# Kernel optimization log

Hardware: AMD Instinct MI355X
Metric: run time of the kernel (lower is better)

The kernel has to match this reference:

```python
import jax, jax.numpy as jnp
import numpy as np

D_MODEL = 1024
EXPAND = 2
D_INNER = D_MODEL * EXPAND  # 2048
C = 8
B, T = 4, 2048


def setup_inputs() -> dict:
    key = jax.random.key(0)
    ks = jax.random.split(key, 8)
    x = jax.random.normal(ks[0], (B, T, D_MODEL), jnp.float32)
    # omega init: uniform in [a, b] per the torch code
    a = np.log(1.0 / np.exp(np.log(0.999) / C) - 1.0)
    b = np.log(1.0 / np.exp(np.log(0.9) / C) - 1.0)
    omega = (a + (b - a) * jax.random.uniform(ks[1], (1, 1, D_INNER))).astype(jnp.float32)
    s = 0.02
    Win = (jax.random.normal(ks[2], (2 * D_INNER, D_MODEL)) * s).astype(jnp.float32)   # in_proj, no bias
    Wl = (jax.random.normal(ks[3], (D_INNER, D_INNER)) * s).astype(jnp.float32)        # lambda_proj weight
    bl = jnp.zeros((D_INNER,), jnp.float32)                                            # lambda_proj bias
    Wv = (jax.random.normal(ks[4], (D_INNER, D_INNER)) * s).astype(jnp.float32)        # mixer householder-vector proj
    bv = jnp.zeros((D_INNER,), jnp.float32)
    Wout = (jax.random.normal(ks[5], (D_MODEL, D_INNER)) * s).astype(jnp.float32)      # out_proj, no bias
    return dict(x=x, omega=omega, Win=Win, Wl=Wl, bl=bl, Wv=Wv, bv=bv, Wout=Wout)


def reference(x, omega, Win, Wl, bl, Wv, bv, Wout):
    # in_proj then split into (x, z)
    xz = jnp.einsum('btd,ed->bte', x, Win)              # [B,T,2*D_INNER]
    xi, z = jnp.split(xz, 2, axis=-1)                   # each [B,T,D_INNER]
    # lambda gate (computed for all timesteps at once)
    log_lam = -C * jax.nn.softplus(omega) * jax.nn.sigmoid(jnp.einsum('bti,ji->btj', xi, Wl) + bl)
    lam = jnp.exp(log_lam)                              # [B,T,D_INNER]
    # Householder (rank-1, identity activation) mixer vectors, hoisted out of the scan
    v = jnp.einsum('bti,ji->btj', xi, Wv) + bv          # [B,T,D_INNER]

    h0 = xi[:, 0]                                       # [B,D_INNER]

    def step(h_prev, inp):
        x_t, v_t, lam_t = inp
        vh = jnp.sum(v_t * h_prev, axis=-1, keepdims=True)
        vv = jnp.sum(v_t * v_t, axis=-1, keepdims=True)
        Qh = h_prev - 2.0 * v_t * (vh / vv)             # Householder reflection of h
        h = lam_t * Qh + (1.0 - lam_t) * x_t
        return h, h

    xs = (jnp.swapaxes(xi[:, 1:], 0, 1),                # [T-1,B,D_INNER]
          jnp.swapaxes(v[:, 1:], 0, 1),
          jnp.swapaxes(lam[:, 1:], 0, 1))
    _, hs = jax.lax.scan(step, h0, xs)                  # [T-1,B,D_INNER]
    h = jnp.concatenate([h0[:, None], jnp.swapaxes(hs, 0, 1)], axis=1)  # [B,T,D_INNER]

    return jnp.einsum('bti,di->btd', jax.nn.silu(z) * h, Wout)
```

## Files before the change

### kernel.cpp

```cpp
#include <hip/hip_runtime.h>
#include <cstdint>
#include <cstddef>

typedef unsigned short u16;
typedef __attribute__((ext_vector_type(8))) short s8v;
typedef __attribute__((ext_vector_type(4))) float f4v;
typedef __attribute__((ext_vector_type(2))) float f32x2;

#define D_MODEL 1024
#define D_INNER 2048
#define BT      8192
#define TLEN    2048
#define NBATCH  4

struct alignas(8) U16x4 { u16 x, y, z, w; };

__device__ __forceinline__ u16 f2bf(float f) {
  union { float f; unsigned u; } c; c.f = f;
  unsigned r = c.u + 0x7FFFu + ((c.u >> 16) & 1u);
  return (u16)(r >> 16);
}
__device__ __forceinline__ float bf2f(u16 b) {
  union { unsigned u; float f; } c; c.u = ((unsigned)b) << 16;
  return c.f;
}
__device__ __forceinline__ float blo(unsigned u) {
  union { unsigned u; float f; } c; c.u = u << 16; return c.f;
}
__device__ __forceinline__ float bhi(unsigned u) {
  union { unsigned u; float f; } c; c.u = u & 0xffff0000u; return c.f;
}
__device__ __forceinline__ unsigned pkbf(float lo, float hi) {
  union { float f; unsigned u; } a, b; a.f = lo; b.f = hi;
#if __has_builtin(__builtin_amdgcn_perm)
  return __builtin_amdgcn_perm(b.u + 0x8000u, a.u + 0x8000u, 0x07060302u);
#else
  return ((b.u + 0x8000u) & 0xffff0000u) | ((a.u + 0x8000u) >> 16);
#endif
}

#define DPPADD(x, ctrl) \
  ((x) + __builtin_bit_cast(float, __builtin_amdgcn_update_dpp( \
       0, __builtin_bit_cast(int, (x)), (ctrl), 0xF, 0xF, true)))
__device__ __forceinline__ float wave_sum_dpp(float x) {
  x = DPPADD(x, 0x111);
  x = DPPADD(x, 0x112);
  x = DPPADD(x, 0x114);
  x = DPPADD(x, 0x118);
  x = DPPADD(x, 0x142);
  x = DPPADD(x, 0x143);
  return x;
}

__device__ __forceinline__ void glds16(const u16* g, const u16* lds) {
  __builtin_amdgcn_global_load_lds(
      (const __attribute__((address_space(1))) unsigned int*)(uintptr_t)g,
      (__attribute__((address_space(3))) unsigned int*)(unsigned int)(uintptr_t)lds,
      16, 0, 0);
}

template<int EPI>
__global__ __launch_bounds__(256, 2)
void gemm_nt(const u16* __restrict__ A, const u16* __restrict__ B,
             int M, int N, int K,
             float* __restrict__ Cf, u16* __restrict__ Cb, u16* __restrict__ Cb2,
             const float* __restrict__ bias, const float* __restrict__ sfac,
             const float* __restrict__ bias2)
{
  __shared__ u16 lA[128 * 32];
  __shared__ u16 lB[128 * 32];
  const int tid  = threadIdx.x;
  const int wave = tid >> 6, lane = tid & 63;
  const int wm = wave >> 1, wn = wave & 1;
  const int bm0 = blockIdx.y * 128, bn0 = blockIdx.x * 128;

  const int srow = lane >> 2;
  const int scol = (lane & 3) * 8;
  const u16* pa0 = A + (size_t)(bm0 + wave * 32 + srow) * K + scol;
  const u16* pa1 = pa0 + (size_t)16 * K;
  const u16* pb0 = B + (size_t)(bn0 + wave * 32 + srow) * K + scol;
  const u16* pb1 = pb0 + (size_t)16 * K;
  u16* la0 = lA + (wave * 32) * 32;
  u16* la1 = la0 + 16 * 32;
  u16* lb0 = lB + (wave * 32) * 32;
  u16* lb1 = lb0 + 16 * 32;

  const int fr = lane & 15, kq = lane >> 4;
  const u16* fA = lA + (wm * 64 + fr) * 32 + kq * 8;
  const u16* fB = lB + (wn * 64 + fr) * 32 + kq * 8;

  f4v acc[4][4];
  const f4v zf = {0.f, 0.f, 0.f, 0.f};
  for (int i = 0; i < 4; ++i)
    for (int j = 0; j < 4; ++j)
      acc[i][j] = zf;

  for (int k0 = 0; k0 < K; k0 += 32) {
    glds16(pa0 + k0, la0);
    glds16(pa1 + k0, la1);
    glds16(pb0 + k0, lb0);
    glds16(pb1 + k0, lb1);
    __syncthreads();
    s8v af[4], bfv[4];
#pragma unroll
    for (int i = 0; i < 4; ++i) af[i] = *(const s8v*)(fA + i * 16 * 32);
#pragma unroll
    for (int j = 0; j < 4; ++j) bfv[j] = *(const s8v*)(fB + j * 16 * 32);
#pragma unroll
    for (int i = 0; i < 4; ++i)
#pragma unroll
      for (int j = 0; j < 4; ++j)
        acc[i][j] = __builtin_amdgcn_mfma_f32_16x16x32_bf16(af[i], bfv[j], acc[i][j], 0, 0, 0);
    __syncthreads();
  }

#pragma unroll
  for (int i = 0; i < 4; ++i) {
#pragma unroll
    for (int j = 0; j < 4; ++j) {
#pragma unroll
      for (int r = 0; r < 4; ++r) {
        const int gm = bm0 + wm * 64 + i * 16 + kq * 4 + r;
        const int gn = bn0 + wn * 64 + j * 16 + fr;
        const float val = acc[i][j][r];
        if (EPI == 0) {
          if (gn < D_INNER) {
            Cb[(size_t)gm * D_INNER + gn] = f2bf(val);
          } else {
            const float s = val / (1.f + __expf(-val));
            Cb2[(size_t)gm * D_INNER + (gn - D_INNER)] = f2bf(s);
          }
        } else if (EPI == 4) {
          if (gn < D_INNER) {
            const float pre = val + bias[gn];
            const float sig = 1.f / (1.f + __expf(-pre));
            Cf[(size_t)gm * D_INNER + gn] = __expf(sfac[gn] * sig);
          } else {
            Cb[(size_t)gm * D_INNER + (gn - D_INNER)] = f2bf(val + bias2[gn - D_INNER]);
          }
        } else {
          Cf[(size_t)gm * N + gn] = val;
        }
      }
    }
  }
}

__global__ void conv_bf16_kernel(const float* __restrict__ in, u16* __restrict__ out, int n4)
{
  const int i = blockIdx.x * blockDim.x + threadIdx.x;
  if (i >= n4) return;
  const float4 x = ((const float4*)in)[i];
  U16x4 o; o.x = f2bf(x.x); o.y = f2bf(x.y); o.z = f2bf(x.z); o.w = f2bf(x.w);
  ((U16x4*)out)[i] = o;
}

__global__ void sfac_kernel(const float* __restrict__ omega, float* __restrict__ sfac)
{
  const int i = blockIdx.x * blockDim.x + threadIdx.x;
  if (i < D_INNER) sfac[i] = -8.f * log1pf(expf(omega[i]));
}

__global__ __launch_bounds__(256)
void vscale_kernel(u16* __restrict__ v)
{
  const int row  = blockIdx.x * 4 + (threadIdx.x >> 6);
  const int lane = threadIdx.x & 63;
  uint4* p = (uint4*)(v + (size_t)row * D_INNER + lane * 32);
  uint4 a[4];
#pragma unroll
  for (int i = 0; i < 4; ++i) a[i] = p[i];
  float s = 0.f;
#pragma unroll
  for (int i = 0; i < 4; ++i) {
    const unsigned w[4] = {a[i].x, a[i].y, a[i].z, a[i].w};
#pragma unroll
    for (int j = 0; j < 4; ++j) {
      const float f0 = blo(w[j]), f1 = bhi(w[j]);
      s += f0 * f0 + f1 * f1;
    }
  }
  s += __shfl_down(s, 32); s += __shfl_down(s, 16); s += __shfl_down(s, 8);
  s += __shfl_down(s, 4);  s += __shfl_down(s, 2);  s += __shfl_down(s, 1);
  const float sc = sqrtf(2.f / __shfl(s, 0));
#pragma unroll
  for (int i = 0; i < 4; ++i) {
    const unsigned w[4] = {a[i].x, a[i].y, a[i].z, a[i].w};
    unsigned o[4];
#pragma unroll
    for (int j = 0; j < 4; ++j) o[j] = pkbf(blo(w[j]) * sc, bhi(w[j]) * sc);
    uint4 ov; ov.x = o[0]; ov.y = o[1]; ov.z = o[2]; ov.w = o[3];
    p[i] = ov;
  }
}

__global__ __launch_bounds__(256)
void pairprep_kernel(const u16* __restrict__ vs, const float* __restrict__ lam,
                     const u16* __restrict__ xi, u16* __restrict__ w,
                     f32x2* __restrict__ C12)
{
  const int r = blockIdx.x * 4 + (threadIdx.x >> 6);
  const int lane = threadIdx.x & 63;
  const int b = r >> 10;
  const int t = (r & 1023) * 2;
  const size_t o0 = ((size_t)b * TLEN + t) * D_INNER + (size_t)lane * 32;
  const size_t o1 = o0 + D_INNER;
  const uint4*  pv0 = (const uint4*)(vs + o0);
  const uint4*  pv1 = (const uint4*)(vs + o1);
  const uint4*  px0 = (const uint4*)(xi + o0);
  const float4* pl0 = (const float4*)(lam + o0);
  uint4* pw = (uint4*)(w + (size_t)r * D_INNER + (size_t)lane * 32);
  float c1 = 0.f, c2 = 0.f;
#pragma unroll
  for (int i = 0; i < 4; ++i) {
    const uint4 v0 = pv0[i], v1 = pv1[i], x0 = px0[i];
    const float4 la = pl0[2 * i], lb2 = pl0[2 * i + 1];
    const unsigned v0w[4] = {v0.x, v0.y, v0.z, v0.w};
    const unsigned v1w[4] = {v1.x, v1.y, v1.z, v1.w};
    const unsigned x0w[4] = {x0.x, x0.y, x0.z, x0.w};
    const float lf[8] = {la.x, la.y, la.z, la.w, lb2.x, lb2.y, lb2.z, lb2.w};
    unsigned ow[4];
#pragma unroll
    for (int q = 0; q < 4; ++q) {
      const float va = blo(v0w[q]), vb = bhi(v0w[q]);
      const float ua = blo(v1w[q]), ub = bhi(v1w[q]);
      const float xa = blo(x0w[q]), xb = bhi(x0w[q]);
      ow[q] = pkbf(ua * lf[2 * q], ub * lf[2 * q + 1]);
      c1 += blo(ow[q]) * va + bhi(ow[q]) * vb;
      c2 += ua * (1.f - lf[2 * q]) * xa + ub * (1.f - lf[2 * q + 1]) * xb;
    }
    uint4 o; o.x = ow[0]; o.y = ow[1]; o.z = ow[2]; o.w = ow[3];
    pw[i] = o;
  }
  c1 = wave_sum_dpp(c1);
  c2 = wave_sum_dpp(c2);
  if (lane == 63) { f32x2 cc; cc.x = c1; cc.y = c2; C12[r] = cc; }
}

struct Pair {
  uint4 v0, v1, w, x0, x1, z0, z1;
  float4 l0a, l0b, l1a, l1b;
  f32x2 c;
};

__global__ __launch_bounds__(256, 1)
void scan2_kernel(const u16* __restrict__ xi, const u16* __restrict__ sz,
                  const u16* __restrict__ vs, const float* __restrict__ lam,
                  const u16* __restrict__ whalf, const f32x2* __restrict__ C12,
                  u16* __restrict__ gh)
{
  const int b = blockIdx.x, tid = threadIdx.x;
  const int wave = tid >> 6, lane = tid & 63;
  const size_t base = (size_t)b * TLEN * D_INNER + (size_t)tid * 8;
  const size_t wb0  = (size_t)(b * 1024) * D_INNER + (size_t)tid * 8;
  const int cb0 = b * 1024;
  __shared__ __attribute__((aligned(16))) float rP[2][4], rQ[2][4];

  auto load_pair = [&](int t) {
    Pair p;
    const size_t o0 = base + (size_t)t * D_INNER;
    const size_t o1 = o0 + D_INNER;
    p.v0 = *(const uint4*)(vs + o0);
    p.v1 = *(const uint4*)(vs + o1);
    p.w  = *(const uint4*)(whalf + wb0 + (size_t)(t >> 1) * D_INNER);
    p.x0 = *(const uint4*)(xi + o0);
    p.x1 = *(const uint4*)(xi + o1);
    p.z0 = *(const uint4*)(sz + o0);
    p.z1 = *(const uint4*)(sz + o1);
    const float4* l0p = (const float4*)(lam + o0);
    p.l0a = l0p[0]; p.l0b = l0p[1];
    const float4* l1p = (const float4*)(lam + o1);
    p.l1a = l1p[0]; p.l1b = l1p[1];
    p.c = C12[cb0 + (t >> 1)];
    return p;
  };

  float h[8];
  {
    const uint4 x0 = *(const uint4*)(xi + base);
    const uint4 z0 = *(const uint4*)(sz + base);
    const unsigned xw[4] = {x0.x, x0.y, x0.z, x0.w};
    const unsigned zw[4] = {z0.x, z0.y, z0.z, z0.w};
    unsigned ow[4];
#pragma unroll
    for (int p = 0; p < 4; ++p) {
      h[2*p]   = blo(xw[p]);
      h[2*p+1] = bhi(xw[p]);
      ow[p] = pkbf(blo(zw[p]) * h[2*p], bhi(zw[p]) * h[2*p+1]);
    }
    uint4 out; out.x = ow[0]; out.y = ow[1]; out.z = ow[2]; out.w = ow[3];
    *(uint4*)(gh + base) = out;
  }

  {
    const size_t o = base + D_INNER;
    const uint4 v1v = *(const uint4*)(vs + o);
    const uint4 x1v = *(const uint4*)(xi + o);
    const uint4 z1v = *(const uint4*)(sz + o);
    const float4* lp = (const float4*)(lam + o);
    const float4 la = lp[0], lb2 = lp[1];
    const unsigned vw[4] = {v1v.x, v1v.y, v1v.z, v1v.w};
    float vf[8];
    float P0 = 0.f, P1 = 0.f;
#pragma unroll
    for (int p = 0; p < 4; ++p) {
      vf[2*p]   = blo(vw[p]);
      vf[2*p+1] = bhi(vw[p]);
      P0 = __builtin_fmaf(vf[2*p],   h[2*p],   P0);
      P1 = __builtin_fmaf(vf[2*p+1], h[2*p+1], P1);
    }
    float P = wave_sum_dpp(P0 + P1);
    if (lane == 63) rP[0][wave] = P;
    asm volatile("s_waitcnt lgkmcnt(0)\n\ts_barrier" ::: "memory");
    const float4 sp = *(const float4*)rP[0];
    const float a = (sp.x + sp.y) + (sp.z + sp.w);
    const float lf[8] = {la.x, la.y, la.z, la.w, lb2.x, lb2.y, lb2.z, lb2.w};
    const unsigned xw[4] = {x1v.x, x1v.y, x1v.z, x1v.w};
    const unsigned zw[4] = {z1v.x, z1v.y, z1v.z, z1v.w};
    unsigned ow[4];
#pragma unroll
    for (int p = 0; p < 4; ++p) {
      const float X0 = blo(xw[p]), X1 = bhi(xw[p]);
      const float t0 = __builtin_fmaf(vf[2*p],   -a, h[2*p]);
      const float t1 = __builtin_fmaf(vf[2*p+1], -a, h[2*p+1]);
      h[2*p]   = __builtin_fmaf(lf[2*p],   t0 - X0, X0);
      h[2*p+1] = __builtin_fmaf(lf[2*p+1], t1 - X1, X1);
      ow[p] = pkbf(blo(zw[p]) * h[2*p], bhi(zw[p]) * h[2*p+1]);
    }
    uint4 out; out.x = ow[0]; out.y = ow[1]; out.z = ow[2]; out.w = ow[3];
    *(uint4*)(gh + o) = out;
  }

  auto round = [&](const Pair& p, int t) {
    const int par = (t >> 1) & 1;
    const unsigned vw[4] = {p.v0.x, p.v0.y, p.v0.z, p.v0.w};
    const unsigned ww[4] = {p.w.x, p.w.y, p.w.z, p.w.w};
    float vf[8];
    float P0 = 0.f, P1 = 0.f, Q0 = 0.f, Q1 = 0.f;
#pragma unroll
    for (int q = 0; q < 4; ++q) {
      vf[2*q]   = blo(vw[q]);
      vf[2*q+1] = bhi(vw[q]);
      const float wa = blo(ww[q]), wb = bhi(ww[q]);
      P0 = __builtin_fmaf(vf[2*q],   h[2*q],   P0);
      P1 = __builtin_fmaf(vf[2*q+1], h[2*q+1], P1);
      Q0 = __builtin_fmaf(wa, h[2*q],   Q0);
      Q1 = __builtin_fmaf(wb, h[2*q+1], Q1);
    }
    float P = wave_sum_dpp(P0 + P1);
    float Q = wave_sum_dpp(Q0 + Q1);
    if (lane == 63) { rP[par][wave] = P; rQ[par][wave] = Q; }
    asm volatile("s_waitcnt lgkmcnt(0)\n\ts_barrier" ::: "memory");
    const float4 sp = *(const float4*)rP[par];
    const float4 sq = *(const float4*)rQ[par];
    const float a0 = (sp.x + sp.y) + (sp.z + sp.w);
    const float a1 = __builtin_fmaf(-a0, p.c.x, (sq.x + sq.y) + (sq.z + sq.w) + p.c.y);
    const float lf0[8] = {p.l0a.x, p.l0a.y, p.l0a.z, p.l0a.w,
                          p.l0b.x, p.l0b.y, p.l0b.z, p.l0b.w};
    const float lf1[8] = {p.l1a.x, p.l1a.y, p.l1a.z, p.l1a.w,
                          p.l1b.x, p.l1b.y, p.l1b.z, p.l1b.w};
    const unsigned v1w[4] = {p.v1.x, p.v1.y, p.v1.z, p.v1.w};
    const unsigned xw0[4] = {p.x0.x, p.x0.y, p.x0.z, p.x0.w};
    const unsigned xw1[4] = {p.x1.x, p.x1.y, p.x1.z, p.x1.w};
    const unsigned zw0[4] = {p.z0.x, p.z0.y, p.z0.z, p.z0.w};
    const unsigned zw1[4] = {p.z1.x, p.z1.y, p.z1.z, p.z1.w};
    unsigned ow0[4], ow1[4];
#pragma unroll
    for (int q = 0; q < 4; ++q) {
      const float A0 = blo(xw0[q]), A1 = bhi(xw0[q]);
      const float B0 = blo(xw1[q]), B1 = bhi(xw1[q]);
      float t0 = __builtin_fmaf(vf[2*q],   -a0, h[2*q]);
      float t1 = __builtin_fmaf(vf[2*q+1], -a0, h[2*q+1]);
      t0 = __builtin_fmaf(lf0[2*q],   t0 - A0, A0);
      t1 = __builtin_fmaf(lf0[2*q+1], t1 - A1, A1);
      ow0[q] = pkbf(blo(zw0[q]) * t0, bhi(zw0[q]) * t1);
      const float u0 = __builtin_fmaf(blo(v1w[q]), -a1, t0);
      const float u1 = __builtin_fmaf(bhi(v1w[q]), -a1, t1);
      h[2*q]   = __builtin_fmaf(lf1[2*q],   u0 - B0, B0);
      h[2*q+1] = __builtin_fmaf(lf1[2*q+1], u1 - B1, B1);
      ow1[q] = pkbf(blo(zw1[q]) * h[2*q], bhi(zw1[q]) * h[2*q+1]);
    }
    const size_t oo = base + (size_t)t * D_INNER;
    uint4 o0; o0.x = ow0[0]; o0.y = ow0[1]; o0.z = ow0[2]; o0.w = ow0[3];
    uint4 o1; o1.x = ow1[0]; o1.y = ow1[1]; o1.z = ow1[2]; o1.w = ow1[3];
    *(uint4*)(gh + oo) = o0;
    *(uint4*)(gh + oo + D_INNER) = o1;
  };

  Pair A = load_pair(2);
  __builtin_amdgcn_sched_barrier(0);
  Pair B = load_pair(4);
  __builtin_amdgcn_sched_barrier(0);
  for (int t = 2; t <= 2038; t += 4) {
    Pair An = load_pair(t + 4);
    __builtin_amdgcn_sched_barrier(0);
    round(A, t);
    A = An;
    Pair Bn = load_pair(t + 6);
    __builtin_amdgcn_sched_barrier(0);
    round(B, t + 2);
    B = Bn;
  }
  {
    Pair An = load_pair(2046);
    __builtin_amdgcn_sched_barrier(0);
    round(A, 2042);
    round(B, 2044);
    round(An, 2046);
  }
}

extern "C" void kernel_launch(void* const* d_in, const int* in_sizes, int n_in,
                              void* d_out, int out_size, void* d_ws, size_t ws_size,
                              hipStream_t stream)
{
  const float* x     = (const float*)d_in[0];
  const float* omega = (const float*)d_in[1];
  const float* Win   = (const float*)d_in[2];
  const float* Wl    = (const float*)d_in[3];
  const float* bl    = (const float*)d_in[4];
  const float* Wv    = (const float*)d_in[5];
  const float* bv    = (const float*)d_in[6];
  const float* Wout  = (const float*)d_in[7];
  float* out = (float*)d_out;
  (void)in_sizes; (void)n_in; (void)out_size; (void)ws_size;

  size_t off = 0;
  auto carve = [&](size_t bytes) -> void* {
    void* r = (char*)d_ws + off;
    off += (bytes + 255) & ~(size_t)255;
    return r;
  };
  u16*  x_bf    = (u16*)carve((size_t)BT * D_MODEL * 2);
  u16*  Win_bf  = (u16*)carve((size_t)2 * D_INNER * D_MODEL * 2);
  u16*  Wl_bf   = (u16*)carve((size_t)D_INNER * D_INNER * 2);
  u16*  Wv_bf   = (u16*)carve((size_t)D_INNER * D_INNER * 2);
  u16*  Wout_bf = (u16*)carve((size_t)D_MODEL * D_INNER * 2);
  u16*  xi_bf   = (u16*)carve((size_t)BT * D_INNER * 2);
  u16*  sz_bf   = (u16*)carve((size_t)BT * D_INNER * 2);
  u16*  v_bf    = (u16*)carve((size_t)BT * D_INNER * 2);
  u16*  gh_bf   = (u16*)carve((size_t)BT * D_INNER * 2);
  float* lam    = (float*)carve((size_t)BT * D_INNER * 4);
  float* sfac   = (float*)carve((size_t)D_INNER * 4);
  f32x2* C12    = (f32x2*)carve((size_t)(BT / 2) * 8);
  u16*  whalf   = x_bf;

  conv_bf16_kernel<<<(BT * D_MODEL / 4 + 255) / 256, 256, 0, stream>>>(x, x_bf, BT * D_MODEL / 4);
  conv_bf16_kernel<<<(2 * D_INNER * D_MODEL / 4 + 255) / 256, 256, 0, stream>>>(Win, Win_bf, 2 * D_INNER * D_MODEL / 4);
  conv_bf16_kernel<<<(D_INNER * D_INNER / 4 + 255) / 256, 256, 0, stream>>>(Wl, Wl_bf, D_INNER * D_INNER / 4);
  conv_bf16_kernel<<<(D_INNER * D_INNER / 4 + 255) / 256, 256, 0, stream>>>(Wv, Wv_bf, D_INNER * D_INNER / 4);
  conv_bf16_kernel<<<(D_MODEL * D_INNER / 4 + 255) / 256, 256, 0, stream>>>(Wout, Wout_bf, D_MODEL * D_INNER / 4);
  sfac_kernel<<<(D_INNER + 255) / 256, 256, 0, stream>>>(omega, sfac);

  gemm_nt<0><<<dim3(4096 / 128, BT / 128), 256, 0, stream>>>(
      x_bf, Win_bf, BT, 4096, D_MODEL, nullptr, xi_bf, sz_bf, nullptr, nullptr, nullptr);
  gemm_nt<4><<<dim3(4096 / 128, BT / 128), 256, 0, stream>>>(
      xi_bf, Wl_bf, BT, 4096, D_INNER, lam, v_bf, nullptr, bl, sfac, bv);
  vscale_kernel<<<BT / 4, 256, 0, stream>>>(v_bf);
  pairprep_kernel<<<BT / 2 / 4, 256, 0, stream>>>(v_bf, lam, xi_bf, whalf, C12);
  scan2_kernel<<<NBATCH, 256, 0, stream>>>(xi_bf, sz_bf, v_bf, lam, whalf, C12, gh_bf);
  gemm_nt<3><<<dim3(D_MODEL / 128, BT / 128), 256, 0, stream>>>(
      gh_bf, Wout_bf, BT, D_MODEL, D_INNER, out, nullptr, nullptr, nullptr, nullptr, nullptr);
}
```

Before: 1.265 ms.

## Shrink scan memory traffic: bf16 one-minus-lambda, drop w buffer, move z-gate out

The lambda GEMM epilogue now stores m = 1 - lambda (via -expm1) as bf16 instead of fp32 lambda, which halves that buffer. The serial scan no longer reads z, fp32 lambda or the precomputed w buffer; it rebuilds w from v1 and m in registers and writes raw h. A new elementwise zmul kernel applies the silu(z) gate afterwards. The aim is to cut per-step bytes loaded in the latency-bound 4-block scan, at the cost of an extra full pass over gh and sz and some bf16 rounding of m.

```diff
diff --git a/kernel.cpp b/kernel.cpp
--- a/kernel.cpp
+++ b/kernel.cpp
@@ -19,10 +19,6 @@
   union { float f; unsigned u; } c; c.f = f;
   unsigned r = c.u + 0x7FFFu + ((c.u >> 16) & 1u);
   return (u16)(r >> 16);
-}
-__device__ __forceinline__ float bf2f(u16 b) {
-  union { unsigned u; float f; } c; c.u = ((unsigned)b) << 16;
-  return c.f;
 }
 __device__ __forceinline__ float blo(unsigned u) {
   union { unsigned u; float f; } c; c.u = u << 16; return c.f;
@@ -134,7 +130,8 @@
           if (gn < D_INNER) {
             const float pre = val + bias[gn];
             const float sig = 1.f / (1.f + __expf(-pre));
-            Cf[(size_t)gm * D_INNER + gn] = __expf(sfac[gn] * sig);
+            const float m = -expm1f(sfac[gn] * sig);
+            Cb2[(size_t)gm * D_INNER + gn] = f2bf(m);
           } else {
             Cb[(size_t)gm * D_INNER + (gn - D_INNER)] = f2bf(val + bias2[gn - D_INNER]);
           }
@@ -195,9 +192,8 @@
 }
 
 __global__ __launch_bounds__(256)
-void pairprep_kernel(const u16* __restrict__ vs, const float* __restrict__ lam,
-                     const u16* __restrict__ xi, u16* __restrict__ w,
-                     f32x2* __restrict__ C12)
+void pairprep_kernel(const u16* __restrict__ vs, const u16* __restrict__ mb,
+                     const u16* __restrict__ xi, f32x2* __restrict__ C12)
 {
   const int r = blockIdx.x * 4 + (threadIdx.x >> 6);
   const int lane = threadIdx.x & 63;
@@ -205,54 +201,64 @@
   const int t = (r & 1023) * 2;
   const size_t o0 = ((size_t)b * TLEN + t) * D_INNER + (size_t)lane * 32;
   const size_t o1 = o0 + D_INNER;
-  const uint4*  pv0 = (const uint4*)(vs + o0);
-  const uint4*  pv1 = (const uint4*)(vs + o1);
-  const uint4*  px0 = (const uint4*)(xi + o0);
-  const float4* pl0 = (const float4*)(lam + o0);
-  uint4* pw = (uint4*)(w + (size_t)r * D_INNER + (size_t)lane * 32);
+  const uint4* pv0 = (const uint4*)(vs + o0);
+  const uint4* pv1 = (const uint4*)(vs + o1);
+  const uint4* px0 = (const uint4*)(xi + o0);
+  const uint4* pm0 = (const uint4*)(mb + o0);
   float c1 = 0.f, c2 = 0.f;
 #pragma unroll
   for (int i = 0; i < 4; ++i) {
-    const uint4 v0 = pv0[i], v1 = pv1[i], x0 = px0[i];
-    const float4 la = pl0[2 * i], lb2 = pl0[2 * i + 1];
+    const uint4 v0 = pv0[i], v1 = pv1[i], x0 = px0[i], m0 = pm0[i];
     const unsigned v0w[4] = {v0.x, v0.y, v0.z, v0.w};
     const unsigned v1w[4] = {v1.x, v1.y, v1.z, v1.w};
     const unsigned x0w[4] = {x0.x, x0.y, x0.z, x0.w};
-    const float lf[8] = {la.x, la.y, la.z, la.w, lb2.x, lb2.y, lb2.z, lb2.w};
-    unsigned ow[4];
+    const unsigned m0w[4] = {m0.x, m0.y, m0.z, m0.w};
 #pragma unroll
     for (int q = 0; q < 4; ++q) {
       const float va = blo(v0w[q]), vb = bhi(v0w[q]);
       const float ua = blo(v1w[q]), ub = bhi(v1w[q]);
       const float xa = blo(x0w[q]), xb = bhi(x0w[q]);
-      ow[q] = pkbf(ua * lf[2 * q], ub * lf[2 * q + 1]);
-      c1 += blo(ow[q]) * va + bhi(ow[q]) * vb;
-      c2 += ua * (1.f - lf[2 * q]) * xa + ub * (1.f - lf[2 * q + 1]) * xb;
-    }
-    uint4 o; o.x = ow[0]; o.y = ow[1]; o.z = ow[2]; o.w = ow[3];
-    pw[i] = o;
+      const float ma = blo(m0w[q]), mbv = bhi(m0w[q]);
+      const float wa = __builtin_fmaf(-ua, ma, ua);
+      const float wb = __builtin_fmaf(-ub, mbv, ub);
+      c1 += wa * va + wb * vb;
+      c2 += ua * (ma * xa) + ub * (mbv * xb);
+    }
   }
   c1 = wave_sum_dpp(c1);
   c2 = wave_sum_dpp(c2);
   if (lane == 63) { f32x2 cc; cc.x = c1; cc.y = c2; C12[r] = cc; }
 }
 
+__global__ void zmul_kernel(u16* __restrict__ gh, const u16* __restrict__ sz, int n8)
+{
+  const int i = blockIdx.x * blockDim.x + threadIdx.x;
+  if (i >= n8) return;
+  const uint4 hv = ((const uint4*)gh)[i];
+  const uint4 zv = ((const uint4*)sz)[i];
+  const unsigned hw[4] = {hv.x, hv.y, hv.z, hv.w};
+  const unsigned zw[4] = {zv.x, zv.y, zv.z, zv.w};
+  unsigned ow[4];
+#pragma unroll
+  for (int q = 0; q < 4; ++q)
+    ow[q] = pkbf(blo(zw[q]) * blo(hw[q]), bhi(zw[q]) * bhi(hw[q]));
+  uint4 o; o.x = ow[0]; o.y = ow[1]; o.z = ow[2]; o.w = ow[3];
+  ((uint4*)gh)[i] = o;
+}
+
 struct Pair {
-  uint4 v0, v1, w, x0, x1, z0, z1;
-  float4 l0a, l0b, l1a, l1b;
+  uint4 v0, v1, x0, x1, m0, m1;
   f32x2 c;
 };
 
 __global__ __launch_bounds__(256, 1)
-void scan2_kernel(const u16* __restrict__ xi, const u16* __restrict__ sz,
-                  const u16* __restrict__ vs, const float* __restrict__ lam,
-                  const u16* __restrict__ whalf, const f32x2* __restrict__ C12,
-                  u16* __restrict__ gh)
+void scan2_kernel(const u16* __restrict__ xi, const u16* __restrict__ vs,
+                  const u16* __restrict__ mb, const f32x2* __restrict__ C12,
+                  u16* __restrict__ hb)
 {
   const int b = blockIdx.x, tid = threadIdx.x;
   const int wave = tid >> 6, lane = tid & 63;
   const size_t base = (size_t)b * TLEN * D_INNER + (size_t)tid * 8;
-  const size_t wb0  = (size_t)(b * 1024) * D_INNER + (size_t)tid * 8;
   const int cb0 = b * 1024;
   __shared__ __attribute__((aligned(16))) float rP[2][4], rQ[2][4];
 
@@ -262,15 +268,10 @@
     const size_t o1 = o0 + D_INNER;
     p.v0 = *(const uint4*)(vs + o0);
     p.v1 = *(const uint4*)(vs + o1);
-    p.w  = *(const uint4*)(whalf + wb0 + (size_t)(t >> 1) * D_INNER);
     p.x0 = *(const uint4*)(xi + o0);
     p.x1 = *(const uint4*)(xi + o1);
-    p.z0 = *(const uint4*)(sz + o0);
-    p.z1 = *(const uint4*)(sz + o1);
-    const float4* l0p = (const float4*)(lam + o0);
-    p.l0a = l0p[0]; p.l0b = l0p[1];
-    const float4* l1p = (const float4*)(lam + o1);
-    p.l1a = l1p[0]; p.l1b = l1p[1];
+    p.m0 = *(const uint4*)(mb + o0);
+    p.m1 = *(const uint4*)(mb + o1);
     p.c = C12[cb0 + (t >> 1)];
     return p;
   };
@@ -278,27 +279,20 @@
   float h[8];
   {
     const uint4 x0 = *(const uint4*)(xi + base);
-    const uint4 z0 = *(const uint4*)(sz + base);
     const unsigned xw[4] = {x0.x, x0.y, x0.z, x0.w};
-    const unsigned zw[4] = {z0.x, z0.y, z0.z, z0.w};
-    unsigned ow[4];
 #pragma unroll
     for (int p = 0; p < 4; ++p) {
       h[2*p]   = blo(xw[p]);
       h[2*p+1] = bhi(xw[p]);
-      ow[p] = pkbf(blo(zw[p]) * h[2*p], bhi(zw[p]) * h[2*p+1]);
-    }
-    uint4 out; out.x = ow[0]; out.y = ow[1]; out.z = ow[2]; out.w = ow[3];
-    *(uint4*)(gh + base) = out;
+    }
+    *(uint4*)(hb + base) = x0;
   }
 
   {
     const size_t o = base + D_INNER;
     const uint4 v1v = *(const uint4*)(vs + o);
     const uint4 x1v = *(const uint4*)(xi + o);
-    const uint4 z1v = *(const uint4*)(sz + o);
-    const float4* lp = (const float4*)(lam + o);
-    const float4 la = lp[0], lb2 = lp[1];
+    const uint4 m1v = *(const uint4*)(mb + o);
     const unsigned vw[4] = {v1v.x, v1v.y, v1v.z, v1v.w};
     float vf[8];
     float P0 = 0.f, P1 = 0.f;
@@ -314,34 +308,40 @@
     asm volatile("s_waitcnt lgkmcnt(0)\n\ts_barrier" ::: "memory");
     const float4 sp = *(const float4*)rP[0];
     const float a = (sp.x + sp.y) + (sp.z + sp.w);
-    const float lf[8] = {la.x, la.y, la.z, la.w, lb2.x, lb2.y, lb2.z, lb2.w};
     const unsigned xw[4] = {x1v.x, x1v.y, x1v.z, x1v.w};
-    const unsigned zw[4] = {z1v.x, z1v.y, z1v.z, z1v.w};
+    const unsigned mw[4] = {m1v.x, m1v.y, m1v.z, m1v.w};
     unsigned ow[4];
 #pragma unroll
     for (int p = 0; p < 4; ++p) {
       const float X0 = blo(xw[p]), X1 = bhi(xw[p]);
+      const float M0 = blo(mw[p]), M1 = bhi(mw[p]);
       const float t0 = __builtin_fmaf(vf[2*p],   -a, h[2*p]);
       const float t1 = __builtin_fmaf(vf[2*p+1], -a, h[2*p+1]);
-      h[2*p]   = __builtin_fmaf(lf[2*p],   t0 - X0, X0);
-      h[2*p+1] = __builtin_fmaf(lf[2*p+1], t1 - X1, X1);
-      ow[p] = pkbf(blo(zw[p]) * h[2*p], bhi(zw[p]) * h[2*p+1]);
+      h[2*p]   = __builtin_fmaf(M0, X0 - t0, t0);
+      h[2*p+1] = __builtin_fmaf(M1, X1 - t1, t1);
+      ow[p] = pkbf(h[2*p], h[2*p+1]);
     }
     uint4 out; out.x = ow[0]; out.y = ow[1]; out.z = ow[2]; out.w = ow[3];
-    *(uint4*)(gh + o) = out;
+    *(uint4*)(hb + o) = out;
   }
 
   auto round = [&](const Pair& p, int t) {
     const int par = (t >> 1) & 1;
-    const unsigned vw[4] = {p.v0.x, p.v0.y, p.v0.z, p.v0.w};
-    const unsigned ww[4] = {p.w.x, p.w.y, p.w.z, p.w.w};
-    float vf[8];
+    const unsigned v0w[4] = {p.v0.x, p.v0.y, p.v0.z, p.v0.w};
+    const unsigned v1w[4] = {p.v1.x, p.v1.y, p.v1.z, p.v1.w};
+    const unsigned m0w[4] = {p.m0.x, p.m0.y, p.m0.z, p.m0.w};
+    float vf[8], uf[8], mf0[8];
     float P0 = 0.f, P1 = 0.f, Q0 = 0.f, Q1 = 0.f;
 #pragma unroll
     for (int q = 0; q < 4; ++q) {
-      vf[2*q]   = blo(vw[q]);
-      vf[2*q+1] = bhi(vw[q]);
-      const float wa = blo(ww[q]), wb = bhi(ww[q]);
+      vf[2*q]   = blo(v0w[q]);
+      vf[2*q+1] = bhi(v0w[q]);
+      uf[2*q]   = blo(v1w[q]);
+      uf[2*q+1] = bhi(v1w[q]);
+      mf0[2*q]  = blo(m0w[q]);
+      mf0[2*q+1]= bhi(m0w[q]);
+      const float wa = __builtin_fmaf(-uf[2*q],   mf0[2*q],   uf[2*q]);
+      const float wb = __builtin_fmaf(-uf[2*q+1], mf0[2*q+1], uf[2*q+1]);
       P0 = __builtin_fmaf(vf[2*q],   h[2*q],   P0);
       P1 = __builtin_fmaf(vf[2*q+1], h[2*q+1], P1);
       Q0 = __builtin_fmaf(wa, h[2*q],   Q0);
@@ -355,36 +355,31 @@
     const float4 sq = *(const float4*)rQ[par];
     const float a0 = (sp.x + sp.y) + (sp.z + sp.w);
     const float a1 = __builtin_fmaf(-a0, p.c.x, (sq.x + sq.y) + (sq.z + sq.w) + p.c.y);
-    const float lf0[8] = {p.l0a.x, p.l0a.y, p.l0a.z, p.l0a.w,
-                          p.l0b.x, p.l0b.y, p.l0b.z, p.l0b.w};
-    const float lf1[8] = {p.l1a.x, p.l1a.y, p.l1a.z, p.l1a.w,
-                          p.l1b.x, p.l1b.y, p.l1b.z, p.l1b.w};
-    const unsigned v1w[4] = {p.v1.x, p.v1.y, p.v1.z, p.v1.w};
     const unsigned xw0[4] = {p.x0.x, p.x0.y, p.x0.z, p.x0.w};
     const unsigned xw1[4] = {p.x1.x, p.x1.y, p.x1.z, p.x1.w};
-    const unsigned zw0[4] = {p.z0.x, p.z0.y, p.z0.z, p.z0.w};
-    const unsigned zw1[4] = {p.z1.x, p.z1.y, p.z1.z, p.z1.w};
+    const unsigned m1w[4] = {p.m1.x, p.m1.y, p.m1.z, p.m1.w};
     unsigned ow0[4], ow1[4];
 #pragma unroll
     for (int q = 0; q < 4; ++q) {
       const float A0 = blo(xw0[q]), A1 = bhi(xw0[q]);
       const float B0 = blo(xw1[q]), B1 = bhi(xw1[q]);
+      const float N0 = blo(m1w[q]), N1 = bhi(m1w[q]);
       float t0 = __builtin_fmaf(vf[2*q],   -a0, h[2*q]);
       float t1 = __builtin_fmaf(vf[2*q+1], -a0, h[2*q+1]);
-      t0 = __builtin_fmaf(lf0[2*q],   t0 - A0, A0);
-      t1 = __builtin_fmaf(lf0[2*q+1], t1 - A1, A1);
-      ow0[q] = pkbf(blo(zw0[q]) * t0, bhi(zw0[q]) * t1);
-      const float u0 = __builtin_fmaf(blo(v1w[q]), -a1, t0);
-      const float u1 = __builtin_fmaf(bhi(v1w[q]), -a1, t1);
-      h[2*q]   = __builtin_fmaf(lf1[2*q],   u0 - B0, B0);
-      h[2*q+1] = __builtin_fmaf(lf1[2*q+1], u1 - B1, B1);
-      ow1[q] = pkbf(blo(zw1[q]) * h[2*q], bhi(zw1[q]) * h[2*q+1]);
+      t0 = __builtin_fmaf(mf0[2*q],   A0 - t0, t0);
+      t1 = __builtin_fmaf(mf0[2*q+1], A1 - t1, t1);
+      ow0[q] = pkbf(t0, t1);
+      const float u0 = __builtin_fmaf(uf[2*q],   -a1, t0);
+      const float u1 = __builtin_fmaf(uf[2*q+1], -a1, t1);
+      h[2*q]   = __builtin_fmaf(N0, B0 - u0, u0);
+      h[2*q+1] = __builtin_fmaf(N1, B1 - u1, u1);
+      ow1[q] = pkbf(h[2*q], h[2*q+1]);
     }
     const size_t oo = base + (size_t)t * D_INNER;
     uint4 o0; o0.x = ow0[0]; o0.y = ow0[1]; o0.z = ow0[2]; o0.w = ow0[3];
     uint4 o1; o1.x = ow1[0]; o1.y = ow1[1]; o1.z = ow1[2]; o1.w = ow1[3];
-    *(uint4*)(gh + oo) = o0;
-    *(uint4*)(gh + oo + D_INNER) = o1;
+    *(uint4*)(hb + oo) = o0;
+    *(uint4*)(hb + oo + D_INNER) = o1;
   };
 
   Pair A = load_pair(2);
@@ -440,10 +435,9 @@
   u16*  sz_bf   = (u16*)carve((size_t)BT * D_INNER * 2);
   u16*  v_bf    = (u16*)carve((size_t)BT * D_INNER * 2);
   u16*  gh_bf   = (u16*)carve((size_t)BT * D_INNER * 2);
-  float* lam    = (float*)carve((size_t)BT * D_INNER * 4);
+  u16*  mb      = (u16*)carve((size_t)BT * D_INNER * 2);
   float* sfac   = (float*)carve((size_t)D_INNER * 4);
   f32x2* C12    = (f32x2*)carve((size_t)(BT / 2) * 8);
-  u16*  whalf   = x_bf;
 
   conv_bf16_kernel<<<(BT * D_MODEL / 4 + 255) / 256, 256, 0, stream>>>(x, x_bf, BT * D_MODEL / 4);
   conv_bf16_kernel<<<(2 * D_INNER * D_MODEL / 4 + 255) / 256, 256, 0, stream>>>(Win, Win_bf, 2 * D_INNER * D_MODEL / 4);
@@ -455,10 +449,11 @@
   gemm_nt<0><<<dim3(4096 / 128, BT / 128), 256, 0, stream>>>(
       x_bf, Win_bf, BT, 4096, D_MODEL, nullptr, xi_bf, sz_bf, nullptr, nullptr, nullptr);
   gemm_nt<4><<<dim3(4096 / 128, BT / 128), 256, 0, stream>>>(
-      xi_bf, Wl_bf, BT, 4096, D_INNER, lam, v_bf, nullptr, bl, sfac, bv);
+      xi_bf, Wl_bf, BT, 4096, D_INNER, nullptr, v_bf, mb, bl, sfac, bv);
   vscale_kernel<<<BT / 4, 256, 0, stream>>>(v_bf);
-  pairprep_kernel<<<BT / 2 / 4, 256, 0, stream>>>(v_bf, lam, xi_bf, whalf, C12);
-  scan2_kernel<<<NBATCH, 256, 0, stream>>>(xi_bf, sz_bf, v_bf, lam, whalf, C12, gh_bf);
+  pairprep_kernel<<<BT / 2 / 4, 256, 0, stream>>>(v_bf, mb, xi_bf, C12);
+  scan2_kernel<<<NBATCH, 256, 0, stream>>>(xi_bf, v_bf, mb, C12, gh_bf);
+  zmul_kernel<<<(BT * D_INNER / 8 + 255) / 256, 256, 0, stream>>>(gh_bf, sz_bf, BT * D_INNER / 8);
   gemm_nt<3><<<dim3(D_MODEL / 128, BT / 128), 256, 0, stream>>>(
       gh_bf, Wout_bf, BT, D_MODEL, D_INNER, out, nullptr, nullptr, nullptr, nullptr, nullptr);
 }
```

Result: faster. 1.088 ms (-14.0%).
